# Optimization experiments

Hardware: AMD Instinct MI355X
Metric: run time of the kernel (lower is better)

The kernel has to match this reference:

```python
import jax, jax.numpy as jnp
import numpy as np

N = 50000   # nodes
E = 800000  # edges
HID = 160   # hidden_dim = 32*5
LM = 768    # lm_input_dim
SUB = 32    # hidden_dim / 5


def setup_inputs() -> dict:
    key = jax.random.key(0)
    ks = iter(jax.random.split(key, 64))

    def rn(shape, s=1.0):
        return jax.random.normal(next(ks), shape, jnp.float32) * s

    def lin(din, dout):
        s = 1.0 / np.sqrt(din)
        return rn((dout, din), s), rn((dout,), s)

    inp = {
        'pre_x': rn((N, LM)),
        'x': rn((N, HID)),  # unused by forward (overwritten), kept for signature fidelity
        'num_prop': rn((N, 6)),
        'num_category': rn((N, 11)),
        'des_tensor': rn((N, LM)),
        'tweet_tensor': rn((N, LM)),
        'edge_index': jax.random.randint(next(ks), (2, E), 0, N, dtype=jnp.int32),
        'edge_type': jax.random.randint(next(ks), (E,), 0, 3, dtype=jnp.int32),
    }
    inp['w_np'], inp['b_np'] = lin(6, SUB)
    inp['w_nc'], inp['b_nc'] = lin(11, SUB)
    inp['w_des'], inp['b_des'] = lin(LM, SUB)
    inp['w_text'], inp['b_text'] = lin(LM, SUB)
    inp['w_tw'], inp['b_tw'] = lin(LM, SUB)
    inp['w_in'], inp['b_in'] = lin(HID, HID)
    inp['W1'], inp['b1'] = lin(HID, HID)
    inp['as1'] = rn((HID,), 0.1)
    inp['ad1'] = rn((HID,), 0.1)
    inp['W2'], inp['b2'] = lin(HID, HID)
    inp['as2'] = rn((HID,), 0.1)
    inp['ad2'] = rn((HID,), 0.1)
    inp['w_o1'], inp['b_o1'] = lin(HID, 80)
    inp['w_o2'], inp['b_o2'] = lin(80, 2)
    return inp


def gat_conv(h_in, src, dst, W, b, att_src, att_dst):
    # PyG GATConv, heads=1, negative_slope=0.2, self-loops already in src/dst.
    n = h_in.shape[0]
    h = h_in @ W.T                                   # [N, HID]
    a_s = (h * att_src).sum(-1)                      # [N]
    a_d = (h * att_dst).sum(-1)                      # [N]
    e = jax.nn.leaky_relu(a_s[src] + a_d[dst], 0.2)  # [E]
    m = jax.ops.segment_max(e, dst, num_segments=n)  # per-destination softmax
    ex = jnp.exp(e - m[dst])
    z = jax.ops.segment_sum(ex, dst, num_segments=n)
    alpha = ex / (z[dst] + 1e-16)
    out = jax.ops.segment_sum(h[src] * alpha[:, None], dst, num_segments=n)
    return out + b


def reference(pre_x, x, num_prop, num_category, des_tensor, tweet_tensor,
              edge_index, edge_type,
              w_np, b_np, w_nc, b_nc, w_des, b_des, w_text, b_text, w_tw, b_tw,
              w_in, b_in, W1, b1, as1, ad1, W2, b2, as2, ad2,
              w_o1, b_o1, w_o2, b_o2):
    # dropout is identity (eval mode); nn.LeakyReLU default slope = 0.01
    lrelu = lambda v: jax.nn.leaky_relu(v, 0.01)
    nv = lrelu(num_prop @ w_np.T + b_np)
    cv = lrelu(num_category @ w_nc.T + b_nc)
    dv = lrelu(des_tensor @ w_des.T + b_des)
    tv = lrelu(tweet_tensor @ w_text.T + b_text)
    pv = lrelu(pre_x @ w_tw.T + b_tw)
    h = jnp.concatenate([nv, cv, dv, tv, pv], axis=1)   # [N, HID]
    h = lrelu(h @ w_in.T + b_in)
    n = h.shape[0]
    loops = jnp.arange(n, dtype=edge_index.dtype)        # add_self_loops=True
    src = jnp.concatenate([edge_index[0], loops])
    dst = jnp.concatenate([edge_index[1], loops])
    h = gat_conv(h, src, dst, W1, b1, as1, ad1)
    h = gat_conv(h, src, dst, W2, b2, as2, ad2)
    em = lrelu(h @ w_o1.T + b_o1)                        # [N, 80]
    out = em @ w_o2.T + b_o2                             # [N, 2]
    return (out, em)
```

## Files before the change

kernel.cpp:

```cpp
#include <hip/hip_runtime.h>
#include <hip/hip_bf16.h>

static __device__ __forceinline__ float lrelu01(float v) { return v > 0.0f ? v : 0.01f * v; }

__global__ __launch_bounds__(256) void k_proj(
    const float* __restrict__ pre_x,
    const float* __restrict__ num_prop,
    const float* __restrict__ num_cat,
    const float* __restrict__ des,
    const float* __restrict__ tweet,
    const float* __restrict__ w_np, const float* __restrict__ b_np,
    const float* __restrict__ w_nc, const float* __restrict__ b_nc,
    const float* __restrict__ w_des, const float* __restrict__ b_des,
    const float* __restrict__ w_text, const float* __restrict__ b_text,
    const float* __restrict__ w_tw, const float* __restrict__ b_tw,
    float* __restrict__ h0, int n)
{
  const int node = blockIdx.x * 256 + threadIdx.x;
  if (node >= n) return;
  const int seg = blockIdx.y;

  const float* x; const float* w; const float* b; int din;
  switch (seg) {
    case 0:  x = num_prop; w = w_np;   b = b_np;   din = 6;   break;
    case 1:  x = num_cat;  w = w_nc;   b = b_nc;   din = 11;  break;
    case 2:  x = des;      w = w_des;  b = b_des;  din = 768; break;
    case 3:  x = tweet;    w = w_text; b = b_text; din = 768; break;
    default: x = pre_x;    w = w_tw;   b = b_tw;   din = 768; break;
  }

  float acc[32];
  #pragma unroll
  for (int c = 0; c < 32; ++c) acc[c] = 0.0f;

  if (din == 768) {
    const float4* xr = reinterpret_cast<const float4*>(x + (size_t)node * 768);
    for (int kb = 0; kb < 192; ++kb) {
      const float4 xv = xr[kb];
      #pragma unroll
      for (int c = 0; c < 32; ++c) {
        const float4 wv = *reinterpret_cast<const float4*>(w + c * 768 + kb * 4);
        acc[c] = fmaf(xv.x, wv.x, acc[c]);
        acc[c] = fmaf(xv.y, wv.y, acc[c]);
        acc[c] = fmaf(xv.z, wv.z, acc[c]);
        acc[c] = fmaf(xv.w, wv.w, acc[c]);
      }
    }
  } else {
    const float* xr = x + (size_t)node * din;
    for (int k = 0; k < din; ++k) {
      const float xv = xr[k];
      #pragma unroll
      for (int c = 0; c < 32; ++c) acc[c] = fmaf(xv, w[c * din + k], acc[c]);
    }
  }

  float* out = h0 + (size_t)node * 160 + seg * 32;
  #pragma unroll
  for (int c = 0; c < 32; ++c) out[c] = lrelu01(acc[c] + b[c]);
}

__global__ __launch_bounds__(256) void k_lin160(
    const float* __restrict__ x, const float* __restrict__ w,
    const float* __restrict__ bias, float* __restrict__ out,
    int n, int act)
{
  const int node = blockIdx.x * 256 + threadIdx.x;
  if (node >= n) return;
  const int seg = blockIdx.y;
  const float4* xr = reinterpret_cast<const float4*>(x + (size_t)node * 160);

  float acc[32];
  #pragma unroll
  for (int c = 0; c < 32; ++c) acc[c] = 0.0f;

  for (int k4 = 0; k4 < 40; ++k4) {
    const float4 xv = xr[k4];
    #pragma unroll
    for (int c = 0; c < 32; ++c) {
      const float4 wv = *reinterpret_cast<const float4*>(w + (size_t)(seg * 32 + c) * 160 + k4 * 4);
      acc[c] = fmaf(xv.x, wv.x, acc[c]);
      acc[c] = fmaf(xv.y, wv.y, acc[c]);
      acc[c] = fmaf(xv.z, wv.z, acc[c]);
      acc[c] = fmaf(xv.w, wv.w, acc[c]);
    }
  }

  float* o = out + (size_t)node * 160 + seg * 32;
  #pragma unroll
  for (int c = 0; c < 32; ++c) {
    float v = acc[c] + (bias ? bias[seg * 32 + c] : 0.0f);
    if (act) v = lrelu01(v);
    o[c] = v;
  }
}

__global__ __launch_bounds__(256) void k_att(
    const float* __restrict__ h, const float* __restrict__ att_s,
    const float* __restrict__ att_d,
    float* __restrict__ a_s, float* __restrict__ a_d, int n)
{
  const int node = blockIdx.x * 256 + threadIdx.x;
  if (node >= n) return;
  const float4* r = reinterpret_cast<const float4*>(h + (size_t)node * 160);
  float s = 0.0f, d = 0.0f;
  #pragma unroll
  for (int k4 = 0; k4 < 40; ++k4) {
    const float4 v = r[k4];
    const float4 av = reinterpret_cast<const float4*>(att_s)[k4];
    const float4 dv = reinterpret_cast<const float4*>(att_d)[k4];
    s = fmaf(v.x, av.x, fmaf(v.y, av.y, fmaf(v.z, av.z, fmaf(v.w, av.w, s))));
    d = fmaf(v.x, dv.x, fmaf(v.y, dv.y, fmaf(v.z, dv.z, fmaf(v.w, dv.w, d))));
  }
  a_s[node] = s;
  a_d[node] = d;
}

__global__ __launch_bounds__(256) void k_initdeg(int* __restrict__ deg, int n)
{
  const int i = blockIdx.x * 256 + threadIdx.x;
  if (i < n) deg[i] = 1;
}

__global__ __launch_bounds__(256) void k_count(
    const int* __restrict__ ei, int e, int* __restrict__ deg)
{
  const int i = blockIdx.x * 256 + threadIdx.x;
  if (i < e) atomicAdd(deg + ei[e + i], 1);
}

__global__ __launch_bounds__(256) void k_scan(
    const int* __restrict__ deg, int* __restrict__ row_start,
    int* __restrict__ cursor, int n)
{
  __shared__ int part[256];
  const int t = threadIdx.x;
  const int chunk = (n + 255) / 256;
  const int lo = t * chunk;
  const int hi = min(lo + chunk, n);
  int s = 0;
  for (int i = lo; i < hi; ++i) s += deg[i];
  part[t] = s;
  __syncthreads();
  for (int off = 1; off < 256; off <<= 1) {
    int v = (t >= off) ? part[t - off] : 0;
    __syncthreads();
    part[t] += v;
    __syncthreads();
  }
  int base = (t == 0) ? 0 : part[t - 1];
  for (int i = lo; i < hi; ++i) {
    row_start[i] = base;
    cursor[i] = base;
    base += deg[i];
  }
  if (t == 0) row_start[n] = part[255];
}

__global__ __launch_bounds__(256) void k_scatter(
    const int* __restrict__ ei, int e, int n,
    int* __restrict__ cursor, int* __restrict__ csr_src)
{
  const int i = blockIdx.x * 256 + threadIdx.x;
  const int total = e + n;
  if (i >= total) return;
  int s, d;
  if (i < e) { s = ei[i]; d = ei[e + i]; }
  else       { s = i - e; d = s; }
  const int slot = atomicAdd(cursor + d, 1);
  csr_src[slot] = s;
}

__global__ __launch_bounds__(256) void k_gather(
    const int* __restrict__ row_start, const int* __restrict__ csr_src,
    const float* __restrict__ h, const float* __restrict__ a_s,
    const float* __restrict__ a_d, const float* __restrict__ bias,
    float* __restrict__ out, int n)
{
  const int d = blockIdx.x * 4 + (threadIdx.x >> 6);
  if (d >= n) return;
  const int lane = threadIdx.x & 63;
  const int beg = row_start[d];
  const int end = row_start[d + 1];
  const float ad = a_d[d];

  float z = 0.0f, acc0 = 0.0f, acc1 = 0.0f, acc2 = 0.0f;
  const bool has2 = lane < 32;

  for (int s = beg; s < end; ++s) {
    const int src = csr_src[s];
    float e = a_s[src] + ad;
    e = e > 0.0f ? e : 0.2f * e;
    const float ex = expf(e);
    z += ex;
    const float* hr = h + (size_t)src * 160;
    acc0 = fmaf(ex, hr[lane], acc0);
    acc1 = fmaf(ex, hr[lane + 64], acc1);
    if (has2) acc2 = fmaf(ex, hr[lane + 128], acc2);
  }

  const float inv = 1.0f / (z + 1e-16f);
  float* o = out + (size_t)d * 160;
  o[lane]      = fmaf(acc0, inv, bias[lane]);
  o[lane + 64] = fmaf(acc1, inv, bias[lane + 64]);
  if (has2) o[lane + 128] = fmaf(acc2, inv, bias[lane + 128]);
}

__global__ __launch_bounds__(256) void k_out(
    const float* __restrict__ h,
    const float* __restrict__ w1, const float* __restrict__ b1,
    const float* __restrict__ w2, const float* __restrict__ b2,
    float* __restrict__ out2, float* __restrict__ em, int n)
{
  const int node = blockIdx.x * 256 + threadIdx.x;
  if (node >= n) return;
  const float4* xr = reinterpret_cast<const float4*>(h + (size_t)node * 160);

  float acc[80];
  #pragma unroll
  for (int c = 0; c < 80; ++c) acc[c] = 0.0f;

  for (int k4 = 0; k4 < 40; ++k4) {
    const float4 xv = xr[k4];
    #pragma unroll
    for (int c = 0; c < 80; ++c) {
      const float4 wv = *reinterpret_cast<const float4*>(w1 + (size_t)c * 160 + k4 * 4);
      acc[c] = fmaf(xv.x, wv.x, acc[c]);
      acc[c] = fmaf(xv.y, wv.y, acc[c]);
      acc[c] = fmaf(xv.z, wv.z, acc[c]);
      acc[c] = fmaf(xv.w, wv.w, acc[c]);
    }
  }

  float o0 = b2[0], o1 = b2[1];
  float* emr = em + (size_t)node * 80;
  #pragma unroll
  for (int c4 = 0; c4 < 20; ++c4) {
    float4 v;
    v.x = lrelu01(acc[c4 * 4 + 0] + b1[c4 * 4 + 0]);
    v.y = lrelu01(acc[c4 * 4 + 1] + b1[c4 * 4 + 1]);
    v.z = lrelu01(acc[c4 * 4 + 2] + b1[c4 * 4 + 2]);
    v.w = lrelu01(acc[c4 * 4 + 3] + b1[c4 * 4 + 3]);
    *reinterpret_cast<float4*>(emr + c4 * 4) = v;
    o0 = fmaf(v.x, w2[c4 * 4 + 0], fmaf(v.y, w2[c4 * 4 + 1],
         fmaf(v.z, w2[c4 * 4 + 2], fmaf(v.w, w2[c4 * 4 + 3], o0))));
    o1 = fmaf(v.x, w2[80 + c4 * 4 + 0], fmaf(v.y, w2[80 + c4 * 4 + 1],
         fmaf(v.z, w2[80 + c4 * 4 + 2], fmaf(v.w, w2[80 + c4 * 4 + 3], o1))));
  }
  out2[(size_t)node * 2 + 0] = o0;
  out2[(size_t)node * 2 + 1] = o1;
}

extern "C" void kernel_launch(void* const* d_in, const int* in_sizes, int n_in,
                              void* d_out, int out_size, void* d_ws, size_t ws_size,
                              hipStream_t stream)
{
  const float* pre_x    = (const float*)d_in[0];
  const float* num_prop = (const float*)d_in[2];
  const float* num_cat  = (const float*)d_in[3];
  const float* des      = (const float*)d_in[4];
  const float* tweet    = (const float*)d_in[5];
  const int*   ei       = (const int*)d_in[6];
  const float* w_np  = (const float*)d_in[8];  const float* b_np  = (const float*)d_in[9];
  const float* w_nc  = (const float*)d_in[10]; const float* b_nc  = (const float*)d_in[11];
  const float* w_des = (const float*)d_in[12]; const float* b_des = (const float*)d_in[13];
  const float* w_text= (const float*)d_in[14]; const float* b_text= (const float*)d_in[15];
  const float* w_tw  = (const float*)d_in[16]; const float* b_tw  = (const float*)d_in[17];
  const float* w_in  = (const float*)d_in[18]; const float* b_in  = (const float*)d_in[19];
  const float* W1    = (const float*)d_in[20]; const float* b1    = (const float*)d_in[21];
  const float* as1   = (const float*)d_in[22]; const float* ad1   = (const float*)d_in[23];
  const float* W2    = (const float*)d_in[24]; const float* b2    = (const float*)d_in[25];
  const float* as2   = (const float*)d_in[26]; const float* ad2   = (const float*)d_in[27];
  const float* w_o1  = (const float*)d_in[28]; const float* b_o1  = (const float*)d_in[29];
  const float* w_o2  = (const float*)d_in[30]; const float* b_o2  = (const float*)d_in[31];

  const int n = in_sizes[2] / 6;
  const int e = in_sizes[7];

  float* buf0 = (float*)d_ws;
  float* buf1 = buf0 + (size_t)n * 160;
  float* asb  = buf1 + (size_t)n * 160;
  float* adb  = asb + n;
  int*   deg       = (int*)(adb + n);
  int*   row_start = deg + n;
  int*   cursor    = row_start + (n + 1);
  int*   csr_src   = cursor + n;

  const int nb = (n + 255) / 256;
  const int eb = (e + 255) / 256;
  const int tb = (e + n + 255) / 256;
  const int gb = (n + 3) / 4;

  k_initdeg<<<nb, 256, 0, stream>>>(deg, n);
  k_count<<<eb, 256, 0, stream>>>(ei, e, deg);
  k_scan<<<1, 256, 0, stream>>>(deg, row_start, cursor, n);
  k_scatter<<<tb, 256, 0, stream>>>(ei, e, n, cursor, csr_src);

  k_proj<<<dim3(nb, 5), 256, 0, stream>>>(pre_x, num_prop, num_cat, des, tweet,
      w_np, b_np, w_nc, b_nc, w_des, b_des, w_text, b_text, w_tw, b_tw, buf0, n);
  k_lin160<<<dim3(nb, 5), 256, 0, stream>>>(buf0, w_in, b_in, buf1, n, 1);

  k_lin160<<<dim3(nb, 5), 256, 0, stream>>>(buf1, W1, nullptr, buf0, n, 0);
  k_att<<<nb, 256, 0, stream>>>(buf0, as1, ad1, asb, adb, n);
  k_gather<<<gb, 256, 0, stream>>>(row_start, csr_src, buf0, asb, adb, b1, buf1, n);

  k_lin160<<<dim3(nb, 5), 256, 0, stream>>>(buf1, W2, nullptr, buf0, n, 0);
  k_att<<<nb, 256, 0, stream>>>(buf0, as2, ad2, asb, adb, n);
  k_gather<<<gb, 256, 0, stream>>>(row_start, csr_src, buf0, asb, adb, b2, buf1, n);

  float* out2 = (float*)d_out;
  float* em   = out2 + (size_t)n * 2;
  k_out<<<nb, 256, 0, stream>>>(buf1, w_o1, b_o1, w_o2, b_o2, out2, em, n);
}
```

Baseline: 1.742 ms.

## Split node feature dot-products across 16-lane groups with shuffle reductions

Replaces one-thread-per-node matvecs in the projection, linear, attention and output kernels with 16-lane groups per node. Each group reads contiguous float4 chunks of the row so global loads are coalesced, then reduces the partial sums with xor shuffles. The small num_prop and num_cat projections move into their own segment, and the gather now uses float4 loads and __expf. The cost is many shuffle reductions and extra weight loads per lane, and __expf gives slightly different rounding than expf.

```diff
diff --git a/kernel.cpp b/kernel.cpp
--- a/kernel.cpp
+++ b/kernel.cpp
@@ -2,6 +2,14 @@
 #include <hip/hip_bf16.h>
 
 static __device__ __forceinline__ float lrelu01(float v) { return v > 0.0f ? v : 0.01f * v; }
+
+static __device__ __forceinline__ float dot4(const float4 a, const float4 b, float acc) {
+  acc = fmaf(a.x, b.x, acc);
+  acc = fmaf(a.y, b.y, acc);
+  acc = fmaf(a.z, b.z, acc);
+  acc = fmaf(a.w, b.w, acc);
+  return acc;
+}
 
 __global__ __launch_bounds__(256) void k_proj(
     const float* __restrict__ pre_x,
@@ -16,48 +24,98 @@
     const float* __restrict__ w_tw, const float* __restrict__ b_tw,
     float* __restrict__ h0, int n)
 {
-  const int node = blockIdx.x * 256 + threadIdx.x;
-  if (node >= n) return;
   const int seg = blockIdx.y;
-
-  const float* x; const float* w; const float* b; int din;
-  switch (seg) {
-    case 0:  x = num_prop; w = w_np;   b = b_np;   din = 6;   break;
-    case 1:  x = num_cat;  w = w_nc;   b = b_nc;   din = 11;  break;
-    case 2:  x = des;      w = w_des;  b = b_des;  din = 768; break;
-    case 3:  x = tweet;    w = w_text; b = b_text; din = 768; break;
-    default: x = pre_x;    w = w_tw;   b = b_tw;   din = 768; break;
-  }
-
-  float acc[32];
-  #pragma unroll
-  for (int c = 0; c < 32; ++c) acc[c] = 0.0f;
-
-  if (din == 768) {
-    const float4* xr = reinterpret_cast<const float4*>(x + (size_t)node * 768);
-    for (int kb = 0; kb < 192; ++kb) {
-      const float4 xv = xr[kb];
+  if (seg == 0) {
+    const int node = blockIdx.x * 256 + threadIdx.x;
+    if (node >= n) return;
+    float* o = h0 + (size_t)node * 160;
+    {
+      const float* xr = num_prop + (size_t)node * 6;
+      float xv[6];
+      #pragma unroll
+      for (int k = 0; k < 6; ++k) xv[k] = xr[k];
       #pragma unroll
       for (int c = 0; c < 32; ++c) {
-        const float4 wv = *reinterpret_cast<const float4*>(w + c * 768 + kb * 4);
-        acc[c] = fmaf(xv.x, wv.x, acc[c]);
-        acc[c] = fmaf(xv.y, wv.y, acc[c]);
-        acc[c] = fmaf(xv.z, wv.z, acc[c]);
-        acc[c] = fmaf(xv.w, wv.w, acc[c]);
+        float s = b_np[c];
+        #pragma unroll
+        for (int k = 0; k < 6; ++k) s = fmaf(xv[k], w_np[c * 6 + k], s);
+        o[c] = lrelu01(s);
       }
     }
-  } else {
-    const float* xr = x + (size_t)node * din;
-    for (int k = 0; k < din; ++k) {
-      const float xv = xr[k];
+    {
+      const float* xr = num_cat + (size_t)node * 11;
+      float xv[11];
       #pragma unroll
-      for (int c = 0; c < 32; ++c) acc[c] = fmaf(xv, w[c * din + k], acc[c]);
-    }
-  }
-
-  float* out = h0 + (size_t)node * 160 + seg * 32;
-  #pragma unroll
-  for (int c = 0; c < 32; ++c) out[c] = lrelu01(acc[c] + b[c]);
+      for (int k = 0; k < 11; ++k) xv[k] = xr[k];
+      #pragma unroll
+      for (int c = 0; c < 32; ++c) {
+        float s = b_nc[c];
+        #pragma unroll
+        for (int k = 0; k < 11; ++k) s = fmaf(xv[k], w_nc[c * 11 + k], s);
+        o[32 + c] = lrelu01(s);
+      }
+    }
+    return;
+  }
+
+  const float* x; const float* w; const float* b; int coff;
+  if (seg == 1)      { x = des;   w = w_des;  b = b_des;  coff = 64;  }
+  else if (seg == 2) { x = tweet; w = w_text; b = b_text; coff = 96;  }
+  else               { x = pre_x; w = w_tw;   b = b_tw;   coff = 128; }
+
+  const int t = threadIdx.x;
+  const int wave = t >> 6;
+  const int lane = t & 63;
+  const int grp  = lane >> 4;
+  const int kl   = lane & 15;
+
+  const int node0 = blockIdx.x * 32 + wave * 8 + grp * 2;
+  const int node1 = node0 + 1;
+  const bool ok0 = node0 < n, ok1 = node1 < n;
+  const int m0 = ok0 ? node0 : 0;
+  const int m1 = ok1 ? node1 : 0;
+
+  const float4* x0 = reinterpret_cast<const float4*>(x) + (size_t)m0 * 192 + kl;
+  const float4* x1 = reinterpret_cast<const float4*>(x) + (size_t)m1 * 192 + kl;
+  const float4* wr = reinterpret_cast<const float4*>(w) + kl;
+
+  float a0[32], a1[32];
+  #pragma unroll
+  for (int c = 0; c < 32; ++c) { a0[c] = 0.0f; a1[c] = 0.0f; }
+
+  for (int j = 0; j < 12; ++j) {
+    const float4 xa = x0[j * 16];
+    const float4 xb = x1[j * 16];
+    const float4* wj = wr + j * 16;
+    #pragma unroll
+    for (int c = 0; c < 32; ++c) {
+      const float4 wv = wj[(size_t)c * 192];
+      a0[c] = dot4(xa, wv, a0[c]);
+      a1[c] = dot4(xb, wv, a1[c]);
+    }
+  }
+
+  float v00 = 0.f, v01 = 0.f, v10 = 0.f, v11 = 0.f;
+  #pragma unroll
+  for (int c = 0; c < 32; ++c) {
+    float r0 = a0[c], r1 = a1[c];
+    r0 += __shfl_xor(r0, 1); r0 += __shfl_xor(r0, 2); r0 += __shfl_xor(r0, 4); r0 += __shfl_xor(r0, 8);
+    r1 += __shfl_xor(r1, 1); r1 += __shfl_xor(r1, 2); r1 += __shfl_xor(r1, 4); r1 += __shfl_xor(r1, 8);
+    if (kl == (c & 15)) {
+      if (c < 16) { v00 = r0; v10 = r1; }
+      else        { v01 = r0; v11 = r1; }
+    }
+  }
+
+  const float bl = b[kl], bh = b[kl + 16];
+  if (ok0) {
+    h0[(size_t)node0 * 160 + coff + kl]      = lrelu01(v00 + bl);
+    h0[(size_t)node0 * 160 + coff + 16 + kl] = lrelu01(v01 + bh);
+  }
+  if (ok1) {
+    h0[(size_t)node1 * 160 + coff + kl]      = lrelu01(v10 + bl);
+    h0[(size_t)node1 * 160 + coff + 16 + kl] = lrelu01(v11 + bh);
+  }
 }
 
 __global__ __launch_bounds__(256) void k_lin160(
@@ -65,34 +123,42 @@
     const float* __restrict__ bias, float* __restrict__ out,
     int n, int act)
 {
-  const int node = blockIdx.x * 256 + threadIdx.x;
+  const int t = threadIdx.x;
+  const int wave = t >> 6, lane = t & 63, grp = lane >> 4, kl = lane & 15;
+  const int node = blockIdx.x * 16 + wave * 4 + grp;
   if (node >= n) return;
   const int seg = blockIdx.y;
-  const float4* xr = reinterpret_cast<const float4*>(x + (size_t)node * 160);
+  const bool tail = kl < 8;
+
+  const float4* xr = reinterpret_cast<const float4*>(x) + (size_t)node * 40 + kl;
+  const float4* wr = reinterpret_cast<const float4*>(w) + (size_t)seg * 32 * 40 + kl;
+
+  const float4 xv0 = xr[0];
+  const float4 xv1 = xr[16];
+  float4 xv2 = {0.f, 0.f, 0.f, 0.f};
+  if (tail) xv2 = xr[32];
 
   float acc[32];
   #pragma unroll
-  for (int c = 0; c < 32; ++c) acc[c] = 0.0f;
-
-  for (int k4 = 0; k4 < 40; ++k4) {
-    const float4 xv = xr[k4];
-    #pragma unroll
-    for (int c = 0; c < 32; ++c) {
-      const float4 wv = *reinterpret_cast<const float4*>(w + (size_t)(seg * 32 + c) * 160 + k4 * 4);
-      acc[c] = fmaf(xv.x, wv.x, acc[c]);
-      acc[c] = fmaf(xv.y, wv.y, acc[c]);
-      acc[c] = fmaf(xv.z, wv.z, acc[c]);
-      acc[c] = fmaf(xv.w, wv.w, acc[c]);
-    }
-  }
-
-  float* o = out + (size_t)node * 160 + seg * 32;
-  #pragma unroll
   for (int c = 0; c < 32; ++c) {
-    float v = acc[c] + (bias ? bias[seg * 32 + c] : 0.0f);
-    if (act) v = lrelu01(v);
-    o[c] = v;
-  }
+    float s = dot4(xv0, wr[(size_t)c * 40], 0.0f);
+    s = dot4(xv1, wr[(size_t)c * 40 + 16], s);
+    if (tail) s = dot4(xv2, wr[(size_t)c * 40 + 32], s);
+    acc[c] = s;
+  }
+
+  float v0 = 0.f, v1 = 0.f;
+  #pragma unroll
+  for (int c = 0; c < 32; ++c) {
+    float r = acc[c];
+    r += __shfl_xor(r, 1); r += __shfl_xor(r, 2); r += __shfl_xor(r, 4); r += __shfl_xor(r, 8);
+    if (kl == (c & 15)) { if (c < 16) v0 = r; else v1 = r; }
+  }
+
+  if (bias) { v0 += bias[seg * 32 + kl]; v1 += bias[seg * 32 + 16 + kl]; }
+  if (act) { v0 = lrelu01(v0); v1 = lrelu01(v1); }
+  out[(size_t)node * 160 + seg * 32 + kl]      = v0;
+  out[(size_t)node * 160 + seg * 32 + 16 + kl] = v1;
 }
 
 __global__ __launch_bounds__(256) void k_att(
@@ -100,20 +166,28 @@
     const float* __restrict__ att_d,
     float* __restrict__ a_s, float* __restrict__ a_d, int n)
 {
-  const int node = blockIdx.x * 256 + threadIdx.x;
+  const int t = threadIdx.x;
+  const int wave = t >> 6, lane = t & 63, grp = lane >> 4, kl = lane & 15;
+  const int node = blockIdx.x * 16 + wave * 4 + grp;
   if (node >= n) return;
-  const float4* r = reinterpret_cast<const float4*>(h + (size_t)node * 160);
-  float s = 0.0f, d = 0.0f;
-  #pragma unroll
-  for (int k4 = 0; k4 < 40; ++k4) {
-    const float4 v = r[k4];
-    const float4 av = reinterpret_cast<const float4*>(att_s)[k4];
-    const float4 dv = reinterpret_cast<const float4*>(att_d)[k4];
-    s = fmaf(v.x, av.x, fmaf(v.y, av.y, fmaf(v.z, av.z, fmaf(v.w, av.w, s))));
-    d = fmaf(v.x, dv.x, fmaf(v.y, dv.y, fmaf(v.z, dv.z, fmaf(v.w, dv.w, d))));
-  }
-  a_s[node] = s;
-  a_d[node] = d;
+  const bool tail = kl < 8;
+
+  const float4* xr = reinterpret_cast<const float4*>(h) + (size_t)node * 40 + kl;
+  const float4* as4 = reinterpret_cast<const float4*>(att_s) + kl;
+  const float4* ad4 = reinterpret_cast<const float4*>(att_d) + kl;
+
+  const float4 x0 = xr[0];
+  const float4 x1 = xr[16];
+  float s = dot4(x0, as4[0], 0.0f);  s = dot4(x1, as4[16], s);
+  float d = dot4(x0, ad4[0], 0.0f);  d = dot4(x1, ad4[16], d);
+  if (tail) {
+    const float4 x2 = xr[32];
+    s = dot4(x2, as4[32], s);
+    d = dot4(x2, ad4[32], d);
+  }
+  s += __shfl_xor(s, 1); s += __shfl_xor(s, 2); s += __shfl_xor(s, 4); s += __shfl_xor(s, 8);
+  d += __shfl_xor(d, 1); d += __shfl_xor(d, 2); d += __shfl_xor(d, 4); d += __shfl_xor(d, 8);
+  if (kl == 0) { a_s[node] = s; a_d[node] = d; }
 }
 
 __global__ __launch_bounds__(256) void k_initdeg(int* __restrict__ deg, int n)
@@ -183,27 +257,37 @@
   const int beg = row_start[d];
   const int end = row_start[d + 1];
   const float ad = a_d[d];
-
-  float z = 0.0f, acc0 = 0.0f, acc1 = 0.0f, acc2 = 0.0f;
-  const bool has2 = lane < 32;
+  const bool act = lane < 40;
+  const float4* h4 = reinterpret_cast<const float4*>(h);
+
+  float z = 0.0f;
+  float4 acc = {0.f, 0.f, 0.f, 0.f};
 
   for (int s = beg; s < end; ++s) {
     const int src = csr_src[s];
     float e = a_s[src] + ad;
     e = e > 0.0f ? e : 0.2f * e;
-    const float ex = expf(e);
+    const float ex = __expf(e);
     z += ex;
-    const float* hr = h + (size_t)src * 160;
-    acc0 = fmaf(ex, hr[lane], acc0);
-    acc1 = fmaf(ex, hr[lane + 64], acc1);
-    if (has2) acc2 = fmaf(ex, hr[lane + 128], acc2);
+    if (act) {
+      const float4 hv = h4[(size_t)src * 40 + lane];
+      acc.x = fmaf(ex, hv.x, acc.x);
+      acc.y = fmaf(ex, hv.y, acc.y);
+      acc.z = fmaf(ex, hv.z, acc.z);
+      acc.w = fmaf(ex, hv.w, acc.w);
+    }
   }
 
   const float inv = 1.0f / (z + 1e-16f);
-  float* o = out + (size_t)d * 160;
-  o[lane]      = fmaf(acc0, inv, bias[lane]);
-  o[lane + 64] = fmaf(acc1, inv, bias[lane + 64]);
-  if (has2) o[lane + 128] = fmaf(acc2, inv, bias[lane + 128]);
+  if (act) {
+    const float4 b4 = reinterpret_cast<const float4*>(bias)[lane];
+    float4 o;
+    o.x = fmaf(acc.x, inv, b4.x);
+    o.y = fmaf(acc.y, inv, b4.y);
+    o.z = fmaf(acc.z, inv, b4.z);
+    o.w = fmaf(acc.w, inv, b4.w);
+    reinterpret_cast<float4*>(out)[(size_t)d * 40 + lane] = o;
+  }
 }
 
 __global__ __launch_bounds__(256) void k_out(
@@ -212,43 +296,67 @@
     const float* __restrict__ w2, const float* __restrict__ b2,
     float* __restrict__ out2, float* __restrict__ em, int n)
 {
-  const int node = blockIdx.x * 256 + threadIdx.x;
+  const int t = threadIdx.x;
+  const int wave = t >> 6, lane = t & 63, grp = lane >> 4, kl = lane & 15;
+  const int node = blockIdx.x * 16 + wave * 4 + grp;
   if (node >= n) return;
-  const float4* xr = reinterpret_cast<const float4*>(h + (size_t)node * 160);
+  const bool tail = kl < 8;
+
+  const float4* xr = reinterpret_cast<const float4*>(h) + (size_t)node * 40 + kl;
+  const float4* wr = reinterpret_cast<const float4*>(w1) + kl;
+
+  const float4 xv0 = xr[0];
+  const float4 xv1 = xr[16];
+  float4 xv2 = {0.f, 0.f, 0.f, 0.f};
+  if (tail) xv2 = xr[32];
 
   float acc[80];
   #pragma unroll
-  for (int c = 0; c < 80; ++c) acc[c] = 0.0f;
-
-  for (int k4 = 0; k4 < 40; ++k4) {
-    const float4 xv = xr[k4];
-    #pragma unroll
-    for (int c = 0; c < 80; ++c) {
-      const float4 wv = *reinterpret_cast<const float4*>(w1 + (size_t)c * 160 + k4 * 4);
-      acc[c] = fmaf(xv.x, wv.x, acc[c]);
-      acc[c] = fmaf(xv.y, wv.y, acc[c]);
-      acc[c] = fmaf(xv.z, wv.z, acc[c]);
-      acc[c] = fmaf(xv.w, wv.w, acc[c]);
-    }
-  }
-
-  float o0 = b2[0], o1 = b2[1];
+  for (int c = 0; c < 80; ++c) {
+    float s = dot4(xv0, wr[(size_t)c * 40], 0.0f);
+    s = dot4(xv1, wr[(size_t)c * 40 + 16], s);
+    if (tail) s = dot4(xv2, wr[(size_t)c * 40 + 32], s);
+    acc[c] = s;
+  }
+
+  float e0 = 0.f, e1 = 0.f, e2 = 0.f, e3 = 0.f, e4 = 0.f;
+  #pragma unroll
+  for (int c = 0; c < 80; ++c) {
+    float r = acc[c];
+    r += __shfl_xor(r, 1); r += __shfl_xor(r, 2); r += __shfl_xor(r, 4); r += __shfl_xor(r, 8);
+    if (kl == (c & 15)) {
+      const int slot = c >> 4;
+      if (slot == 0) e0 = r;
+      else if (slot == 1) e1 = r;
+      else if (slot == 2) e2 = r;
+      else if (slot == 3) e3 = r;
+      else e4 = r;
+    }
+  }
+
+  e0 = lrelu01(e0 + b1[kl]);
+  e1 = lrelu01(e1 + b1[kl + 16]);
+  e2 = lrelu01(e2 + b1[kl + 32]);
+  e3 = lrelu01(e3 + b1[kl + 48]);
+  e4 = lrelu01(e4 + b1[kl + 64]);
+
   float* emr = em + (size_t)node * 80;
-  #pragma unroll
-  for (int c4 = 0; c4 < 20; ++c4) {
-    float4 v;
-    v.x = lrelu01(acc[c4 * 4 + 0] + b1[c4 * 4 + 0]);
-    v.y = lrelu01(acc[c4 * 4 + 1] + b1[c4 * 4 + 1]);
-    v.z = lrelu01(acc[c4 * 4 + 2] + b1[c4 * 4 + 2]);
-    v.w = lrelu01(acc[c4 * 4 + 3] + b1[c4 * 4 + 3]);
-    *reinterpret_cast<float4*>(emr + c4 * 4) = v;
-    o0 = fmaf(v.x, w2[c4 * 4 + 0], fmaf(v.y, w2[c4 * 4 + 1],
-         fmaf(v.z, w2[c4 * 4 + 2], fmaf(v.w, w2[c4 * 4 + 3], o0))));
-    o1 = fmaf(v.x, w2[80 + c4 * 4 + 0], fmaf(v.y, w2[80 + c4 * 4 + 1],
-         fmaf(v.z, w2[80 + c4 * 4 + 2], fmaf(v.w, w2[80 + c4 * 4 + 3], o1))));
-  }
-  out2[(size_t)node * 2 + 0] = o0;
-  out2[(size_t)node * 2 + 1] = o1;
+  emr[kl]      = e0;
+  emr[kl + 16] = e1;
+  emr[kl + 32] = e2;
+  emr[kl + 48] = e3;
+  emr[kl + 64] = e4;
+
+  float p0 = e0 * w2[kl] + e1 * w2[kl + 16] + e2 * w2[kl + 32]
+           + e3 * w2[kl + 48] + e4 * w2[kl + 64];
+  float p1 = e0 * w2[80 + kl] + e1 * w2[80 + kl + 16] + e2 * w2[80 + kl + 32]
+           + e3 * w2[80 + kl + 48] + e4 * w2[80 + kl + 64];
+  p0 += __shfl_xor(p0, 1); p0 += __shfl_xor(p0, 2); p0 += __shfl_xor(p0, 4); p0 += __shfl_xor(p0, 8);
+  p1 += __shfl_xor(p1, 1); p1 += __shfl_xor(p1, 2); p1 += __shfl_xor(p1, 4); p1 += __shfl_xor(p1, 8);
+  if (kl == 0) {
+    out2[(size_t)node * 2 + 0] = p0 + b2[0];
+    out2[(size_t)node * 2 + 1] = p1 + b2[1];
+  }
 }
 
 extern "C" void kernel_launch(void* const* d_in, const int* in_sizes, int n_in,
@@ -286,7 +394,9 @@
   int*   cursor    = row_start + (n + 1);
   int*   csr_src   = cursor + n;
 
-  const int nb = (n + 255) / 256;
+  const int nb   = (n + 255) / 256;
+  const int nb32 = (n + 31) / 32;
+  const int nb16 = (n + 15) / 16;
   const int eb = (e + 255) / 256;
   const int tb = (e + n + 255) / 256;
   const int gb = (n + 3) / 4;
@@ -296,19 +406,19 @@
   k_scan<<<1, 256, 0, stream>>>(deg, row_start, cursor, n);
   k_scatter<<<tb, 256, 0, stream>>>(ei, e, n, cursor, csr_src);
 
-  k_proj<<<dim3(nb, 5), 256, 0, stream>>>(pre_x, num_prop, num_cat, des, tweet,
+  k_proj<<<dim3(nb32, 4), 256, 0, stream>>>(pre_x, num_prop, num_cat, des, tweet,
       w_np, b_np, w_nc, b_nc, w_des, b_des, w_text, b_text, w_tw, b_tw, buf0, n);
-  k_lin160<<<dim3(nb, 5), 256, 0, stream>>>(buf0, w_in, b_in, buf1, n, 1);
-
-  k_lin160<<<dim3(nb, 5), 256, 0, stream>>>(buf1, W1, nullptr, buf0, n, 0);
-  k_att<<<nb, 256, 0, stream>>>(buf0, as1, ad1, asb, adb, n);
+  k_lin160<<<dim3(nb16, 5), 256, 0, stream>>>(buf0, w_in, b_in, buf1, n, 1);
+
+  k_lin160<<<dim3(nb16, 5), 256, 0, stream>>>(buf1, W1, nullptr, buf0, n, 0);
+  k_att<<<nb16, 256, 0, stream>>>(buf0, as1, ad1, asb, adb, n);
   k_gather<<<gb, 256, 0, stream>>>(row_start, csr_src, buf0, asb, adb, b1, buf1, n);
 
-  k_lin160<<<dim3(nb, 5), 256, 0, stream>>>(buf1, W2, nullptr, buf0, n, 0);
-  k_att<<<nb, 256, 0, stream>>>(buf0, as2, ad2, asb, adb, n);
+  k_lin160<<<dim3(nb16, 5), 256, 0, stream>>>(buf1, W2, nullptr, buf0, n, 0);
+  k_att<<<nb16, 256, 0, stream>>>(buf0, as2, ad2, asb, adb, n);
   k_gather<<<gb, 256, 0, stream>>>(row_start, csr_src, buf0, asb, adb, b2, buf1, n);
 
   float* out2 = (float*)d_out;
   float* em   = out2 + (size_t)n * 2;
-  k_out<<<nb, 256, 0, stream>>>(buf1, w_o1, b_o1, w_o2, b_o2, out2, em, n);
-}
+  k_out<<<nb16, 256, 0, stream>>>(buf1, w_o1, b_o1, w_o2, b_o2, out2, em, n);
+}
```

After: 2.012 ms. 15.5% more time.
